# Performance work log

Hardware: AMD Instinct MI355X
Metric: run time of the kernel (lower is better)

## Reference

```python
import jax, jax.numpy as jnp
import numpy as np

B, Q, C, H, NSTEPS = 1024, 96, 16, 100, 100  # batch, q (MA order), channels, hidden, Euler steps


def setup_inputs() -> dict:
    key = jax.random.key(0)
    ks = jax.random.split(key, 6)
    s = 0.1  # weight init scale
    return {
        "series": jax.random.normal(ks[0], (B, Q, C), jnp.float32),
        "rand_error": jax.random.normal(ks[1], (B, 1, C), jnp.float32),
        "W1": jax.random.normal(ks[2], (H, Q + 2), jnp.float32) * s,
        "b1": jnp.zeros((H,), jnp.float32),
        "W2": jax.random.normal(ks[3], (H, H), jnp.float32) * s,
        "b2": jnp.zeros((H,), jnp.float32),
        "W3": jax.random.normal(ks[4], (Q + 1, H), jnp.float32) * s,
        "b3": jnp.zeros((Q + 1,), jnp.float32),
    }


def _mlp(x, t, W1, b1, W2, b2, W3, b3):
    # x: (B, Q+1, C), t: (B, 1, C)  -> cat along feature dim, permute to (B, C, Q+2)
    inp = jnp.concatenate([x, t], axis=1).transpose(0, 2, 1)
    h = jnp.tanh(inp @ W1.T + b1)
    h = jnp.tanh(h @ W2.T + b2)
    out = h @ W3.T + b3            # (B, C, Q+1)
    return out.transpose(0, 2, 1)  # (B, Q+1, C)


def reference(series, rand_error, W1, b1, W2, b2, W3, b3):
    # ma_forecast sampling path: noise = cat(series, rand_error) then Euler flow sampling
    noise = jnp.concatenate([series, rand_error], axis=1)  # (B, Q+1, C)
    dt = jnp.float32(1.0 / NSTEPS)

    def step(x, i):
        t = jnp.ones((x.shape[0], 1, x.shape[2]), x.dtype) * (i.astype(x.dtype) / NSTEPS)
        pred = _mlp(x, t, W1, b1, W2, b2, W3, b3)
        return x + (pred - noise) * dt, None

    x, _ = jax.lax.scan(step, noise, jnp.arange(NSTEPS))
    return x
```

## Files before the change

kernel.cpp:

```cpp
#include <hip/hip_runtime.h>


#define NB 1024
#define NQ 96
#define NC 16
#define NH 100
#define QP1 97
#define QP2 98
#define NTHR 256
#define STR 136
#define NSTEPS_ 100
#define MT_K 128

typedef __attribute__((ext_vector_type(8))) short bf16x8;
typedef __attribute__((ext_vector_type(4))) float f32x4;
typedef __attribute__((ext_vector_type(2))) unsigned uintx2;

__device__ __forceinline__ f32x4 splat4(float f) {
  f32x4 v = f;
  return v;
}

__device__ __forceinline__ short f2bf_rne(float f) {
  unsigned u = __builtin_bit_cast(unsigned, f);
  u = u + 0x7fffu + ((u >> 16) & 1u);
  return (short)(u >> 16);
}

__device__ __forceinline__ unsigned pack_bf2(float a, float b) {
  unsigned ua = __builtin_bit_cast(unsigned, a) + 0x8000u;
  unsigned ub = __builtin_bit_cast(unsigned, b) + 0x8000u;
  return __builtin_amdgcn_perm(ub, ua, 0x07060302);
}

__device__ __forceinline__ f32x4 tanh4(f32x4 x) {
  f32x4 u = x * x;
  f32x4 num = x * __builtin_elementwise_fma(u + splat4(105.0f), u, splat4(945.0f));
  f32x4 den = __builtin_elementwise_fma(
      __builtin_elementwise_fma(splat4(15.0f), u, splat4(420.0f)), u,
      splat4(945.0f));
  f32x4 r;
  r[0] = __builtin_amdgcn_rcpf(den[0]);
  r[1] = __builtin_amdgcn_rcpf(den[1]);
  r[2] = __builtin_amdgcn_rcpf(den[2]);
  r[3] = __builtin_amdgcn_rcpf(den[3]);
  f32x4 v = num * r;
  return __builtin_elementwise_min(
      __builtin_elementwise_max(v, splat4(-1.0f)), splat4(1.0f));
}

__global__ void __launch_bounds__(512) arima_prep(
    const float* __restrict__ W1, const float* __restrict__ b1,
    const float* __restrict__ W3, const float* __restrict__ b3,
    short* __restrict__ Mt, float* __restrict__ sv) {
  __shared__ float part[4][128];
  __shared__ float pb[128];
  const int n = blockIdx.x;
  const int tid = threadIdx.x;
  const int k = tid & 127, js = tid >> 7;
  float s = 0.0f;
  if (n < NH && k < NH) {
    int j0 = js * 25, j1 = (js == 3) ? QP1 : j0 + 25;
    for (int j = j0; j < j1; ++j)
      s = fmaf(W1[n * QP2 + j], W3[j * NH + k], s);
  }
  part[js][k] = s;
  if (tid < 128)
    pb[tid] = (tid < QP1 && n < NH) ? W1[n * QP2 + tid] * b3[tid] : 0.0f;
  __syncthreads();
  if (js == 0) {
    float tot = part[0][k] + part[1][k] + part[2][k] + part[3][k];
    Mt[n * MT_K + k] = f2bf_rne(0.01f * tot);
  }
  if (tid == 0) {
    float d = 0.0f;
    for (int j = 0; j < 128; ++j) d += pb[j];
    sv[n] = (n < NH) ? 0.01f * (d + b1[n] + W1[n * QP2 + QP1]) : 0.0f;
  }
}

__device__ void load_afrag(const float* __restrict__ W,
                           const float* __restrict__ bias, int ws, int mvalid,
                           int KW, int m, int quad, bf16x8 dst[4]) {
#pragma unroll
  for (int kb = 0; kb < 4; ++kb) {
    bf16x8 v;
#pragma unroll
    for (int i = 0; i < 8; ++i) {
      int k = kb * 32 + quad * 8 + i;
      float f = 0.0f;
      if (m < mvalid) {
        if (k < KW) f = W[m * ws + k];
        else if (k == KW) f = bias[m];
      }
      v[i] = f2bf_rne(f);
    }
    dst[kb] = v;
  }
}

__device__ __forceinline__ void gemm_acc(const short* __restrict__ src,
                                         int rbase, const bf16x8 (&A)[2][4],
                                         f32x4 (&acc)[2]) {
#pragma unroll
  for (int kb = 0; kb < 4; ++kb) {
    bf16x8 bv = *(const bf16x8*)(src + rbase + kb * 32);
    acc[0] = __builtin_amdgcn_mfma_f32_16x16x32_bf16(A[0][kb], bv, acc[0], 0, 0, 0);
    acc[1] = __builtin_amdgcn_mfma_f32_16x16x32_bf16(A[1][kb], bv, acc[1], 0, 0, 0);
  }
}

__device__ __forceinline__ void write_tiles(short* __restrict__ dst, int wrow,
                                            int T0, int quad, const f32x4& v0,
                                            const f32x4& v1) {
  uintx2 a, b;
  a.x = pack_bf2(v0[0], v0[1]);
  a.y = pack_bf2(v0[2], v0[3]);
  b.x = pack_bf2(v1[0], v1[1]);
  b.y = pack_bf2(v1[2], v1[3]);
  *(uintx2*)(dst + wrow + T0 * 16 + quad * 4) = a;
  *(uintx2*)(dst + wrow + (T0 + 1) * 16 + quad * 4) = b;
}

__global__ void __launch_bounds__(NTHR, 4)
arima_r10(const float* __restrict__ series,
          const float* __restrict__ rand_error, const float* __restrict__ W1,
          const float* __restrict__ b1, const float* __restrict__ W2,
          const float* __restrict__ b2, const float* __restrict__ W3,
          const float* __restrict__ b3, const short* __restrict__ Mt,
          const float* __restrict__ sv, float* __restrict__ out) {
  __shared__ __align__(16) short buf1[16 * STR];
  __shared__ __align__(16) short buf2[16 * STR];

  const int tid = threadIdx.x;
  const int w = tid >> 6, l = tid & 63;
  const int col = l & 15, quad = l >> 4;
  const int b = blockIdx.x;
  const int T0 = 2 * w;
  const int wrow = col * STR;
  const int rbase = wrow + quad * 8;
  const bool fixw = (w == 3 && quad == 1);

  {
    f32x4 xv[2];
#pragma unroll
    for (int t = 0; t < 2; ++t)
#pragma unroll
      for (int r = 0; r < 4; ++r) {
        int q = (T0 + t) * 16 + quad * 4 + r;
        float f = 0.0f;
        if (q < NQ) f = series[(b * NQ + q) * NC + col];
        else if (q == NQ) f = rand_error[b * NC + col];
        else if (q == QP2) f = 1.0f;
        xv[t][r] = f;
      }
    write_tiles(buf2, wrow, T0, quad, xv[0], xv[1]);
  }
  __syncthreads();

  f32x4 z[2], v[2];
  {
    bf16x8 a1[2][4];
#pragma unroll
    for (int t = 0; t < 2; ++t)
      load_afrag(W1, b1, QP2, NH, QP2, (T0 + t) * 16 + col, quad, a1[t]);
    z[0] = splat4(0.0f);
    z[1] = splat4(0.0f);
    gemm_acc(buf2, rbase, a1, z);
#pragma unroll
    for (int t = 0; t < 2; ++t) {
      f32x4 s;
#pragma unroll
      for (int r = 0; r < 4; ++r) s[r] = sv[(T0 + t) * 16 + quad * 4 + r];
      v[t] = s - splat4(0.01f) * z[t];
    }
  }
  {
    f32x4 h0 = tanh4(z[0]), h1 = tanh4(z[1]);
    if (fixw) h0[0] = 1.0f;
    write_tiles(buf1, wrow, T0, quad, h0, h1);
  }
  __syncthreads();

  bf16x8 a2[2][4], am[2][4];
#pragma unroll
  for (int t = 0; t < 2; ++t) {
    load_afrag(W2, b2, NH, NH, NH, (T0 + t) * 16 + col, quad, a2[t]);
#pragma unroll
    for (int kb = 0; kb < 4; ++kb)
      am[t][kb] = *(const bf16x8*)(Mt + ((T0 + t) * 16 + col) * MT_K +
                                   kb * 32 + quad * 8);
  }
  f32x4 h2s[2] = {splat4(0.0f), splat4(0.0f)};

#pragma unroll 1
  for (int step = 0; step < NSTEPS_; ++step) {
    f32x4 acc[2];
    acc[0] = splat4(0.0f);
    acc[1] = splat4(0.0f);
    gemm_acc(buf1, rbase, a2, acc);
    {
      f32x4 h0 = tanh4(acc[0]), h1 = tanh4(acc[1]);
      write_tiles(buf2, wrow, T0, quad, h0, h1);
      h2s[0] = h2s[0] + h0;
      h2s[1] = h2s[1] + h1;
    }
    __syncthreads();
    gemm_acc(buf2, rbase, am, z);
    {
      z[0] = z[0] + v[0];
      z[1] = z[1] + v[1];
      f32x4 h0 = tanh4(z[0]), h1 = tanh4(z[1]);
      if (fixw) h0[0] = 1.0f;
      write_tiles(buf1, wrow, T0, quad, h0, h1);
    }
    __syncthreads();
  }

  {
    f32x4 ha0 = splat4(0.01f) * h2s[0];
    f32x4 ha1 = splat4(0.01f) * h2s[1];
    if (fixw) ha0[0] = 1.0f;
    write_tiles(buf2, wrow, T0, quad, ha0, ha1);
  }
  __syncthreads();
  {
    bf16x8 a3[2][4];
#pragma unroll
    for (int t = 0; t < 2; ++t)
      load_afrag(W3, b3, NH, QP1, NH, (T0 + t) * 16 + col, quad, a3[t]);
    f32x4 o[2];
    o[0] = splat4(0.0f);
    o[1] = splat4(0.0f);
    gemm_acc(buf2, rbase, a3, o);
#pragma unroll
    for (int t = 0; t < 2; ++t)
#pragma unroll
      for (int r = 0; r < 4; ++r) {
        int q = (T0 + t) * 16 + quad * 4 + r;
        if (q < QP1) out[(b * QP1 + q) * NC + col] = o[t][r];
      }
  }
}

extern "C" void kernel_launch(void* const* d_in, const int* in_sizes, int n_in,
                              void* d_out, int out_size, void* d_ws,
                              size_t ws_size, hipStream_t stream) {
  const float* series = (const float*)d_in[0];
  const float* rand_error = (const float*)d_in[1];
  const float* W1 = (const float*)d_in[2];
  const float* b1 = (const float*)d_in[3];
  const float* W2 = (const float*)d_in[4];
  const float* b2 = (const float*)d_in[5];
  const float* W3 = (const float*)d_in[6];
  const float* b3 = (const float*)d_in[7];
  float* out = (float*)d_out;

  short* Mt = (short*)d_ws;
  float* sv = (float*)((char*)d_ws + MT_K * MT_K * 2);

  hipLaunchKernelGGL(arima_prep, dim3(128), dim3(512), 0, stream, W1, b1, W3,
                     b3, Mt, sv);
  hipLaunchKernelGGL(arima_r10, dim3(NB), dim3(NTHR), 0, stream, series,
                     rand_error, W1, b1, W2, b2, W3, b3, Mt, sv, out);
}
```

Baseline: 263.4 us.

## Process two batch elements per block to share weight fragments and barriers

Each workgroup now handles two batch items, interleaving their GEMM chains inside each Euler step so one pair of __syncthreads covers both. The register-held weight fragments (W2 and the folded W3·W1 matrix) are reused across the two items, and the two independent MFMA chains give more instruction-level parallelism, halving barrier count per item. The grid halves to 512 blocks and launch bounds drop to 3 waves per SIMD, which lowers occupancy and may leave CUs underused. tanh clamping also switches to fmed3.

```diff
diff --git a/kernel.cpp b/kernel.cpp
--- a/kernel.cpp
+++ b/kernel.cpp
@@ -35,18 +35,23 @@
 
 __device__ __forceinline__ f32x4 tanh4(f32x4 x) {
   f32x4 u = x * x;
-  f32x4 num = x * __builtin_elementwise_fma(u + splat4(105.0f), u, splat4(945.0f));
+  f32x4 num =
+      x * __builtin_elementwise_fma(u + splat4(105.0f), u, splat4(945.0f));
   f32x4 den = __builtin_elementwise_fma(
       __builtin_elementwise_fma(splat4(15.0f), u, splat4(420.0f)), u,
       splat4(945.0f));
-  f32x4 r;
+  f32x4 r, v;
   r[0] = __builtin_amdgcn_rcpf(den[0]);
   r[1] = __builtin_amdgcn_rcpf(den[1]);
   r[2] = __builtin_amdgcn_rcpf(den[2]);
   r[3] = __builtin_amdgcn_rcpf(den[3]);
-  f32x4 v = num * r;
-  return __builtin_elementwise_min(
-      __builtin_elementwise_max(v, splat4(-1.0f)), splat4(1.0f));
+  v = num * r;
+  f32x4 o;
+  o[0] = __builtin_amdgcn_fmed3f(v[0], -1.0f, 1.0f);
+  o[1] = __builtin_amdgcn_fmed3f(v[1], -1.0f, 1.0f);
+  o[2] = __builtin_amdgcn_fmed3f(v[2], -1.0f, 1.0f);
+  o[3] = __builtin_amdgcn_fmed3f(v[3], -1.0f, 1.0f);
+  return o;
 }
 
 __global__ void __launch_bounds__(512) arima_prep(
@@ -122,26 +127,27 @@
   *(uintx2*)(dst + wrow + (T0 + 1) * 16 + quad * 4) = b;
 }
 
-__global__ void __launch_bounds__(NTHR, 4)
-arima_r10(const float* __restrict__ series,
+__global__ void __launch_bounds__(NTHR, 3)
+arima_r11(const float* __restrict__ series,
           const float* __restrict__ rand_error, const float* __restrict__ W1,
           const float* __restrict__ b1, const float* __restrict__ W2,
           const float* __restrict__ b2, const float* __restrict__ W3,
           const float* __restrict__ b3, const short* __restrict__ Mt,
           const float* __restrict__ sv, float* __restrict__ out) {
-  __shared__ __align__(16) short buf1[16 * STR];
-  __shared__ __align__(16) short buf2[16 * STR];
+  __shared__ __align__(16) short bh1[2][16 * STR];
+  __shared__ __align__(16) short bh2[2][16 * STR];
 
   const int tid = threadIdx.x;
   const int w = tid >> 6, l = tid & 63;
   const int col = l & 15, quad = l >> 4;
-  const int b = blockIdx.x;
+  const int b0 = blockIdx.x * 2;
   const int T0 = 2 * w;
   const int wrow = col * STR;
   const int rbase = wrow + quad * 8;
   const bool fixw = (w == 3 && quad == 1);
 
-  {
+#pragma unroll
+  for (int p = 0; p < 2; ++p) {
     f32x4 xv[2];
 #pragma unroll
     for (int t = 0; t < 2; ++t)
@@ -149,36 +155,37 @@
       for (int r = 0; r < 4; ++r) {
         int q = (T0 + t) * 16 + quad * 4 + r;
         float f = 0.0f;
-        if (q < NQ) f = series[(b * NQ + q) * NC + col];
-        else if (q == NQ) f = rand_error[b * NC + col];
+        if (q < NQ) f = series[((b0 + p) * NQ + q) * NC + col];
+        else if (q == NQ) f = rand_error[(b0 + p) * NC + col];
         else if (q == QP2) f = 1.0f;
         xv[t][r] = f;
       }
-    write_tiles(buf2, wrow, T0, quad, xv[0], xv[1]);
-  }
-  __syncthreads();
-
-  f32x4 z[2], v[2];
+    write_tiles(bh2[p], wrow, T0, quad, xv[0], xv[1]);
+  }
+  __syncthreads();
+
+  f32x4 z[2][2], v[2][2];
   {
     bf16x8 a1[2][4];
 #pragma unroll
     for (int t = 0; t < 2; ++t)
       load_afrag(W1, b1, QP2, NH, QP2, (T0 + t) * 16 + col, quad, a1[t]);
-    z[0] = splat4(0.0f);
-    z[1] = splat4(0.0f);
-    gemm_acc(buf2, rbase, a1, z);
-#pragma unroll
-    for (int t = 0; t < 2; ++t) {
-      f32x4 s;
-#pragma unroll
-      for (int r = 0; r < 4; ++r) s[r] = sv[(T0 + t) * 16 + quad * 4 + r];
-      v[t] = s - splat4(0.01f) * z[t];
-    }
-  }
-  {
-    f32x4 h0 = tanh4(z[0]), h1 = tanh4(z[1]);
-    if (fixw) h0[0] = 1.0f;
-    write_tiles(buf1, wrow, T0, quad, h0, h1);
+    f32x4 s[2];
+#pragma unroll
+    for (int t = 0; t < 2; ++t)
+#pragma unroll
+      for (int r = 0; r < 4; ++r) s[t][r] = sv[(T0 + t) * 16 + quad * 4 + r];
+#pragma unroll
+    for (int p = 0; p < 2; ++p) {
+      z[p][0] = splat4(0.0f);
+      z[p][1] = splat4(0.0f);
+      gemm_acc(bh2[p], rbase, a1, z[p]);
+#pragma unroll
+      for (int t = 0; t < 2; ++t) v[p][t] = s[t] - splat4(0.01f) * z[p][t];
+      f32x4 h0 = tanh4(z[p][0]), h1 = tanh4(z[p][1]);
+      if (fixw) h0[0] = 1.0f;
+      write_tiles(bh1[p], wrow, T0, quad, h0, h1);
+    }
   }
   __syncthreads();
 
@@ -191,37 +198,41 @@
       am[t][kb] = *(const bf16x8*)(Mt + ((T0 + t) * 16 + col) * MT_K +
                                    kb * 32 + quad * 8);
   }
-  f32x4 h2s[2] = {splat4(0.0f), splat4(0.0f)};
+  f32x4 h2s[2][2] = {{splat4(0.0f), splat4(0.0f)},
+                     {splat4(0.0f), splat4(0.0f)}};
 
 #pragma unroll 1
   for (int step = 0; step < NSTEPS_; ++step) {
-    f32x4 acc[2];
-    acc[0] = splat4(0.0f);
-    acc[1] = splat4(0.0f);
-    gemm_acc(buf1, rbase, a2, acc);
-    {
+#pragma unroll
+    for (int p = 0; p < 2; ++p) {
+      f32x4 acc[2];
+      acc[0] = splat4(0.0f);
+      acc[1] = splat4(0.0f);
+      gemm_acc(bh1[p], rbase, a2, acc);
       f32x4 h0 = tanh4(acc[0]), h1 = tanh4(acc[1]);
-      write_tiles(buf2, wrow, T0, quad, h0, h1);
-      h2s[0] = h2s[0] + h0;
-      h2s[1] = h2s[1] + h1;
+      write_tiles(bh2[p], wrow, T0, quad, h0, h1);
+      h2s[p][0] = h2s[p][0] + h0;
+      h2s[p][1] = h2s[p][1] + h1;
     }
     __syncthreads();
-    gemm_acc(buf2, rbase, am, z);
-    {
-      z[0] = z[0] + v[0];
-      z[1] = z[1] + v[1];
-      f32x4 h0 = tanh4(z[0]), h1 = tanh4(z[1]);
+#pragma unroll
+    for (int p = 0; p < 2; ++p) {
+      gemm_acc(bh2[p], rbase, am, z[p]);
+      z[p][0] = z[p][0] + v[p][0];
+      z[p][1] = z[p][1] + v[p][1];
+      f32x4 h0 = tanh4(z[p][0]), h1 = tanh4(z[p][1]);
       if (fixw) h0[0] = 1.0f;
-      write_tiles(buf1, wrow, T0, quad, h0, h1);
+      write_tiles(bh1[p], wrow, T0, quad, h0, h1);
     }
     __syncthreads();
   }
 
-  {
-    f32x4 ha0 = splat4(0.01f) * h2s[0];
-    f32x4 ha1 = splat4(0.01f) * h2s[1];
+#pragma unroll
+  for (int p = 0; p < 2; ++p) {
+    f32x4 ha0 = splat4(0.01f) * h2s[p][0];
+    f32x4 ha1 = splat4(0.01f) * h2s[p][1];
     if (fixw) ha0[0] = 1.0f;
-    write_tiles(buf2, wrow, T0, quad, ha0, ha1);
+    write_tiles(bh2[p], wrow, T0, quad, ha0, ha1);
   }
   __syncthreads();
   {
@@ -229,17 +240,20 @@
 #pragma unroll
     for (int t = 0; t < 2; ++t)
       load_afrag(W3, b3, NH, QP1, NH, (T0 + t) * 16 + col, quad, a3[t]);
-    f32x4 o[2];
-    o[0] = splat4(0.0f);
-    o[1] = splat4(0.0f);
-    gemm_acc(buf2, rbase, a3, o);
-#pragma unroll
-    for (int t = 0; t < 2; ++t)
-#pragma unroll
-      for (int r = 0; r < 4; ++r) {
-        int q = (T0 + t) * 16 + quad * 4 + r;
-        if (q < QP1) out[(b * QP1 + q) * NC + col] = o[t][r];
-      }
+#pragma unroll
+    for (int p = 0; p < 2; ++p) {
+      f32x4 o[2];
+      o[0] = splat4(0.0f);
+      o[1] = splat4(0.0f);
+      gemm_acc(bh2[p], rbase, a3, o);
+#pragma unroll
+      for (int t = 0; t < 2; ++t)
+#pragma unroll
+        for (int r = 0; r < 4; ++r) {
+          int q = (T0 + t) * 16 + quad * 4 + r;
+          if (q < QP1) out[((b0 + p) * QP1 + q) * NC + col] = o[t][r];
+        }
+    }
   }
 }
 
@@ -261,6 +275,6 @@
 
   hipLaunchKernelGGL(arima_prep, dim3(128), dim3(512), 0, stream, W1, b1, W3,
                      b3, Mt, sv);
-  hipLaunchKernelGGL(arima_r10, dim3(NB), dim3(NTHR), 0, stream, series,
+  hipLaunchKernelGGL(arima_r11, dim3(NB / 2), dim3(NTHR), 0, stream, series,
                      rand_error, W1, b1, W2, b2, W3, b3, Mt, sv, out);
 }
```

Result: slower. 279.4 us (+6.1%).
